# Kernel optimization log

Hardware: AMD Instinct MI355X
Metric: run time of the kernel (lower is better)

The kernel has to match this reference:

```python
import jax, jax.numpy as jnp
import numpy as np

N_NODES = 100000
N_EDGES = 3200000
DIM = 64


def setup_inputs() -> dict:
    key = jax.random.key(0)
    k1, k2, k3, k4 = jax.random.split(key, 4)
    features = jax.random.normal(k1, (N_NODES, DIM), dtype=jnp.float32)
    attn_w = jax.random.normal(k2, (2 * DIM,), dtype=jnp.float32) / np.sqrt(2 * DIM)
    src = jax.random.randint(k3, (N_EDGES,), 0, N_NODES, dtype=jnp.int32)
    dst = jax.random.randint(k4, (N_EDGES,), 0, N_NODES, dtype=jnp.int32)
    return {"features": features, "attn_w": attn_w, "src": src, "dst": dst}


def reference(features, attn_w, src, dst):
    n = features.shape[0]
    d = features.shape[1]
    a_src, a_dst = attn_w[:d], attn_w[d:]
    # Edge attention: leaky_relu(Linear(concat(h_src, h_dst))) == leaky_relu(h_src@a_src + h_dst@a_dst)
    s_src = features @ a_src  # [N]
    s_dst = features @ a_dst  # [N]
    e = jax.nn.leaky_relu(s_src[src] + s_dst[dst], negative_slope=0.01)  # [E]
    # Segment softmax over incoming edges of each destination node
    emax = jax.ops.segment_max(e, dst, num_segments=n)  # [N], -inf for isolated nodes
    ee = jnp.exp(e - emax[dst])  # [E]
    denom = jax.ops.segment_sum(ee, dst, num_segments=n)  # [N]
    alpha = ee / denom[dst]  # [E]
    # Weighted neighbor aggregation (gather src feats, scatter-add into dst)
    h = jax.ops.segment_sum(alpha[:, None] * features[src], dst, num_segments=n)  # [N, D]
    return jax.nn.elu(h)
```

## Files before the change

### kernel.cpp

```cpp
#include <hip/hip_runtime.h>
#include <math.h>

#define DIM 64
#define SCAN_BLOCK 1024
#define NB1 1024
#define TPB2 1024
#define BUCKET_BITS 7
#define BUCKET_SZ 128
#define FB_SZ 64
#define SRC_SHIFT 20
#define CAP 6144
#define CAP2 2560
#define CHUNK 12500
#define STAGE_SZ 12544
#define NSPAN 784

__device__ __forceinline__ float lrelu(float x) { return x > 0.f ? x : 0.01f * x; }
__device__ __forceinline__ float elu(float x)  { return x > 0.f ? x : expm1f(x); }

__global__ __launch_bounds__(TPB2)
void prep_scatter(const float* __restrict__ feat,
                  const float* __restrict__ attn_w,
                  float* __restrict__ s_src,
                  float* __restrict__ s_dst,
                  unsigned short* __restrict__ fbf,
                  int n_nodes,
                  const int* __restrict__ src,
                  const int* __restrict__ dst,
                  int* __restrict__ gcur,
                  int* __restrict__ bpk, int m, int nsb) {
    __shared__ int lh[NB1];
    __shared__ int bnd[NB1];
    __shared__ int cur[NB1];
    __shared__ int span_b[NSPAN];
    __shared__ int stage[STAGE_SZ];
    if (blockIdx.x < nsb) {
        int t = threadIdx.x;
        int lo = blockIdx.x * CHUNK;
        int hi = min(m, lo + CHUNK);
        int cc = hi - lo;
        int nbux = (n_nodes + BUCKET_SZ - 1) >> BUCKET_BITS;
        lh[t] = 0;
        __syncthreads();
        for (int i = lo + t; i < hi; i += TPB2)
            atomicAdd(&lh[dst[i] >> BUCKET_BITS], 1);
        __syncthreads();
        cur[t] = lh[t];
        __syncthreads();
        for (int off = 1; off < NB1; off <<= 1) {
            int u = (t >= off) ? cur[t - off] : 0;
            __syncthreads();
            cur[t] += u;
            __syncthreads();
        }
        int excl = cur[t] - lh[t];
        bnd[t] = excl;
        int c = lh[t];
        int gb = (c > 0) ? atomicAdd(&gcur[t], c) : 0;
        lh[t]  = gb;
        cur[t] = excl;
        __syncthreads();
        if (t < nbux) {
            int s0 = (bnd[t] + 15) >> 4;
            int s1 = (bnd[t + 1] + 15) >> 4;
            for (int s = s0; s < s1; ++s) span_b[s] = t;
        }
        for (int i = lo + t; i < hi; i += TPB2) {
            int d = dst[i];
            int b = d >> BUCKET_BITS;
            int p = atomicAdd(&cur[b], 1);
            stage[p] = src[i] | ((d & (BUCKET_SZ - 1)) << SRC_SHIFT);
        }
        __syncthreads();
        for (int j = t; j < cc; j += TPB2) {
            int bkt = span_b[j >> 4];
            while (bnd[bkt + 1] <= j) ++bkt;
            int pos = lh[bkt] + (j - bnd[bkt]);
            if (pos < CAP)
                bpk[(size_t)bkt * CAP + pos] = stage[j];
        }
        return;
    }
    int gid  = (blockIdx.x - nsb) * blockDim.x + threadIdx.x;
    int node = gid >> 4;
    int lane = gid & 15;
    if (node >= n_nodes) return;
    const float4 f  = *reinterpret_cast<const float4*>(feat + (size_t)node * DIM + lane * 4);
    const float4 as = *reinterpret_cast<const float4*>(attn_w + lane * 4);
    const float4 ad = *reinterpret_cast<const float4*>(attn_w + DIM + lane * 4);
    float ps = f.x * as.x + f.y * as.y + f.z * as.z + f.w * as.w;
    float pd = f.x * ad.x + f.y * ad.y + f.z * ad.z + f.w * ad.w;
    uint b0 = __float_as_uint(f.x), b1 = __float_as_uint(f.y);
    uint b2 = __float_as_uint(f.z), b3 = __float_as_uint(f.w);
    ushort4 h;
    h.x = (unsigned short)((b0 + 0x7FFFu + ((b0 >> 16) & 1u)) >> 16);
    h.y = (unsigned short)((b1 + 0x7FFFu + ((b1 >> 16) & 1u)) >> 16);
    h.z = (unsigned short)((b2 + 0x7FFFu + ((b2 >> 16) & 1u)) >> 16);
    h.w = (unsigned short)((b3 + 0x7FFFu + ((b3 >> 16) & 1u)) >> 16);
    *reinterpret_cast<ushort4*>(fbf + (size_t)node * DIM + lane * 4) = h;
    for (int off = 8; off >= 1; off >>= 1) {
        ps += __shfl_xor(ps, off, 16);
        pd += __shfl_xor(pd, off, 16);
    }
    if (lane == 0) {
        s_src[node] = ps;
        s_dst[node] = pd;
    }
}

__device__ __forceinline__ void bf16x8_acc(uint4 q, float w,
                                           float& a0, float& a1, float& a2, float& a3,
                                           float& a4, float& a5, float& a6, float& a7) {
    a0 += w * __uint_as_float(q.x << 16);
    a1 += w * __uint_as_float(q.x & 0xffff0000u);
    a2 += w * __uint_as_float(q.y << 16);
    a3 += w * __uint_as_float(q.y & 0xffff0000u);
    a4 += w * __uint_as_float(q.z << 16);
    a5 += w * __uint_as_float(q.z & 0xffff0000u);
    a6 += w * __uint_as_float(q.w << 16);
    a7 += w * __uint_as_float(q.w & 0xffff0000u);
}

__global__ __launch_bounds__(256)
void sort_aggregate64(const int* __restrict__ bpk,
                      const int* __restrict__ gcur,
                      const float* __restrict__ s_src,
                      const float* __restrict__ s_dst,
                      const unsigned short* __restrict__ fbf,
                      float* __restrict__ out,
                      int n) {
    __shared__ float sdd[FB_SZ];
    __shared__ int   hist[FB_SZ];
    __shared__ int   offsl[FB_SZ];
    __shared__ int   cur[FB_SZ];
    __shared__ int   sA[FB_SZ];
    __shared__ int   sB[FB_SZ];
    __shared__ int   esrc_l[CAP2];
    __shared__ float w_l[CAP2];
    int f = blockIdx.x, t = threadIdx.x;
    int cb = f >> 1;
    int hb = (f & 1) << 6;
    int base = f * FB_SZ;
    int cnt = min(gcur[cb], CAP);
    const int*  bp  = bpk + (size_t)cb * CAP;
    const uint4* bp4 = reinterpret_cast<const uint4*>(bp);
    int cnt4 = cnt >> 2;
    if (t < FB_SZ) {
        hist[t] = 0;
        int nd = base + t;
        sdd[t] = (nd < n) ? s_dst[nd] : 0.f;
    }
    __syncthreads();
#define HPROC(pk) { int dl7_ = ((pk) >> SRC_SHIFT) & 127; \
    if ((dl7_ & 64) == hb) atomicAdd(&hist[dl7_ & 63], 1); }
    for (int e = t; e < cnt4; e += 256) {
        uint4 v = bp4[e];
        HPROC((int)v.x) HPROC((int)v.y) HPROC((int)v.z) HPROC((int)v.w)
    }
    for (int e = (cnt4 << 2) + t; e < cnt; e += 256)
        HPROC(bp[e])
    __syncthreads();
    if (t < FB_SZ) sA[t] = hist[t];
    __syncthreads();
    {
        int* pin = sA; int* pout = sB;
        for (int off = 1; off < FB_SZ; off <<= 1) {
            if (t < FB_SZ) pout[t] = (t >= off) ? pin[t] + pin[t - off] : pin[t];
            __syncthreads();
            int* tmpp = pin; pin = pout; pout = tmpp;
        }
        if (t < FB_SZ) {
            int excl = min(pin[t] - hist[t], CAP2);
            offsl[t] = excl;
            cur[t] = excl;
        }
    }
    __syncthreads();
#define SPROC(pk) { int dl7_ = ((pk) >> SRC_SHIFT) & 127; \
    if ((dl7_ & 64) == hb) { \
        int sv_ = (pk) & ((1 << SRC_SHIFT) - 1); \
        float w_ = __expf(lrelu(s_src[sv_] + sdd[dl7_ & 63])); \
        int p_ = atomicAdd(&cur[dl7_ & 63], 1); \
        if (p_ < CAP2) { esrc_l[p_] = sv_; w_l[p_] = w_; } } }
    for (int e = t; e < cnt4; e += 256) {
        uint4 v = bp4[e];
        SPROC((int)v.x) SPROC((int)v.y) SPROC((int)v.z) SPROC((int)v.w)
    }
    for (int e = (cnt4 << 2) + t; e < cnt; e += 256)
        SPROC(bp[e])
    __syncthreads();
    int l8 = t & 7, grp = t >> 3;
    const uint4* fv4 = reinterpret_cast<const uint4*>(fbf);
    for (int node = grp; node < FB_SZ; node += 32) {
        int st = offsl[node];
        int en = min(st + hist[node], CAP2);
        float a0 = 0.f, a1 = 0.f, a2 = 0.f, a3 = 0.f;
        float a4 = 0.f, a5 = 0.f, a6 = 0.f, a7 = 0.f;
        float wsum = 0.f;
        int e = st;
        for (; e + 4 <= en; e += 4) {
            int   s0 = esrc_l[e],     s1 = esrc_l[e + 1];
            int   s2 = esrc_l[e + 2], s3 = esrc_l[e + 3];
            float w0 = w_l[e],        w1 = w_l[e + 1];
            float w2 = w_l[e + 2],    w3 = w_l[e + 3];
            uint4 q0 = fv4[(size_t)s0 * 8 + l8];
            uint4 q1 = fv4[(size_t)s1 * 8 + l8];
            uint4 q2 = fv4[(size_t)s2 * 8 + l8];
            uint4 q3 = fv4[(size_t)s3 * 8 + l8];
            wsum += (w0 + w1) + (w2 + w3);
            bf16x8_acc(q0, w0, a0, a1, a2, a3, a4, a5, a6, a7);
            bf16x8_acc(q1, w1, a0, a1, a2, a3, a4, a5, a6, a7);
            bf16x8_acc(q2, w2, a0, a1, a2, a3, a4, a5, a6, a7);
            bf16x8_acc(q3, w3, a0, a1, a2, a3, a4, a5, a6, a7);
        }
        for (; e < en; e++) {
            int   s0 = esrc_l[e];
            float w0 = w_l[e];
            uint4 q0 = fv4[(size_t)s0 * 8 + l8];
            wsum += w0;
            bf16x8_acc(q0, w0, a0, a1, a2, a3, a4, a5, a6, a7);
        }
        int nd = base + node;
        if (nd < n) {
            float inv = (en > st) ? 1.f / wsum : 0.f;
            float4 o1, o2;
            o1.x = elu(a0 * inv); o1.y = elu(a1 * inv);
            o1.z = elu(a2 * inv); o1.w = elu(a3 * inv);
            o2.x = elu(a4 * inv); o2.y = elu(a5 * inv);
            o2.z = elu(a6 * inv); o2.w = elu(a7 * inv);
            float4* orow = reinterpret_cast<float4*>(out + (size_t)nd * DIM + l8 * 8);
            orow[0] = o1;
            orow[1] = o2;
        }
    }
#undef HPROC
#undef SPROC
}

__global__ void compute_scores(const float* __restrict__ feat,
                               const float* __restrict__ attn_w,
                               float* __restrict__ s_src,
                               float* __restrict__ s_dst,
                               int n_nodes) {
    int gid  = blockIdx.x * blockDim.x + threadIdx.x;
    int node = gid >> 4;
    int lane = gid & 15;
    if (node >= n_nodes) return;
    const float4 f  = *reinterpret_cast<const float4*>(feat + (size_t)node * DIM + lane * 4);
    const float4 as = *reinterpret_cast<const float4*>(attn_w + lane * 4);
    const float4 ad = *reinterpret_cast<const float4*>(attn_w + DIM + lane * 4);
    float ps = f.x * as.x + f.y * as.y + f.z * as.z + f.w * as.w;
    float pd = f.x * ad.x + f.y * ad.y + f.z * ad.z + f.w * ad.w;
    for (int off = 8; off >= 1; off >>= 1) {
        ps += __shfl_xor(ps, off, 16);
        pd += __shfl_xor(pd, off, 16);
    }
    if (lane == 0) { s_src[node] = ps; s_dst[node] = pd; }
}

__global__ void scan_level1(const int* __restrict__ in, int* __restrict__ out,
                            int* __restrict__ bsum, int n) {
    __shared__ int tmp[SCAN_BLOCK];
    int t = threadIdx.x;
    int g = blockIdx.x * SCAN_BLOCK + t;
    int v = (g < n) ? in[g] : 0;
    tmp[t] = v;
    __syncthreads();
    for (int off = 1; off < SCAN_BLOCK; off <<= 1) {
        int u = (t >= off) ? tmp[t - off] : 0;
        __syncthreads();
        tmp[t] += u;
        __syncthreads();
    }
    if (g < n) out[g] = tmp[t] - v;
    if (t == SCAN_BLOCK - 1) bsum[blockIdx.x] = tmp[t];
}

__global__ void scan_level2(int* __restrict__ bsum, int nb) {
    __shared__ int tmp[SCAN_BLOCK];
    int t = threadIdx.x;
    int v = (t < nb) ? bsum[t] : 0;
    tmp[t] = v;
    __syncthreads();
    for (int off = 1; off < SCAN_BLOCK; off <<= 1) {
        int u = (t >= off) ? tmp[t - off] : 0;
        __syncthreads();
        tmp[t] += u;
        __syncthreads();
    }
    if (t < nb) bsum[t] = tmp[t] - v;
}

__global__ void scan_level3(int* __restrict__ out, const int* __restrict__ bsum,
                            int n) {
    int g = blockIdx.x * SCAN_BLOCK + threadIdx.x;
    if (g < n) out[g] += bsum[blockIdx.x];
}

__global__ void degree_rank(const int* __restrict__ dst, int* __restrict__ deg,
                            int* __restrict__ rank, int m) {
    int i = blockIdx.x * blockDim.x + threadIdx.x;
    if (i >= m) return;
    rank[i] = atomicAdd(&deg[dst[i]], 1);
}

__global__ void scatter_src(const int* __restrict__ src, const int* __restrict__ dst,
                            const int* __restrict__ rank, const int* __restrict__ offs,
                            int* __restrict__ esrc, int m) {
    int i = blockIdx.x * blockDim.x + threadIdx.x;
    if (i >= m) return;
    esrc[offs[dst[i]] + rank[i]] = src[i];
}

__global__ void aggregate_f32(const int* __restrict__ esrc,
                              const int* __restrict__ offs,
                              const int* __restrict__ deg,
                              const float* __restrict__ s_src,
                              const float* __restrict__ s_dst,
                              const float* __restrict__ feat,
                              float* __restrict__ out, int n) {
    int gid  = blockIdx.x * blockDim.x + threadIdx.x;
    int node = gid >> 4;
    int lane = gid & 15;
    if (node >= n) return;
    int start = offs[node];
    int cnt   = deg[node];
    float sdd = s_dst[node];
    const float4* fv = reinterpret_cast<const float4*>(feat);
    float4 acc = {0.f, 0.f, 0.f, 0.f};
    float wsum = 0.f;
    for (int e = 0; e < cnt; e++) {
        int s0 = esrc[start + e];
        float w0 = __expf(lrelu(s_src[s0] + sdd));
        float4 f0 = fv[s0 * 16 + lane];
        wsum += w0;
        acc.x += w0 * f0.x; acc.y += w0 * f0.y;
        acc.z += w0 * f0.z; acc.w += w0 * f0.w;
    }
    float inv = (cnt > 0) ? 1.f / wsum : 0.f;
    float4 o;
    o.x = elu(acc.x * inv); o.y = elu(acc.y * inv);
    o.z = elu(acc.z * inv); o.w = elu(acc.w * inv);
    reinterpret_cast<float4*>(out)[node * 16 + lane] = o;
}

extern "C" void kernel_launch(void* const* d_in, const int* in_sizes, int n_in,
                              void* d_out, int out_size, void* d_ws, size_t ws_size,
                              hipStream_t stream) {
    const float* feat   = (const float*)d_in[0];
    const float* attn_w = (const float*)d_in[1];
    const int*   src    = (const int*)d_in[2];
    const int*   dst    = (const int*)d_in[3];

    const int n = in_sizes[0] / DIM;
    const int m = in_sizes[2];

    float* out = (float*)d_out;

    const int nbux = (n + BUCKET_SZ - 1) >> BUCKET_BITS;
    const int nfb  = (n + FB_SZ - 1) / FB_SZ;

    float* s_src = (float*)d_ws;
    float* s_dst = s_src + n;
    unsigned short* fbf = (unsigned short*)(s_dst + n);
    int*   gcur  = (int*)(fbf + (size_t)n * DIM);
    int*   bpk   = gcur + NB1;
    size_t need  = ((size_t)(2 + DIM / 2) * n + NB1 + (size_t)nbux * CAP)
                   * sizeof(int);

    if (ws_size >= need && nbux <= NB1) {
        hipMemsetAsync(gcur, 0, (size_t)NB1 * sizeof(int), stream);

        int nsb = (m + CHUNK - 1) / CHUNK;
        int PB  = (n * 16 + TPB2 - 1) / TPB2;
        prep_scatter<<<nsb + PB, TPB2, 0, stream>>>(
            feat, attn_w, s_src, s_dst, fbf, n, src, dst, gcur, bpk, m, nsb);

        sort_aggregate64<<<nfb, 256, 0, stream>>>(
            bpk, gcur, s_src, s_dst, fbf, out, n);
    } else {
        int* deg2  = (int*)(s_dst + n);
        int* offs2 = deg2 + n;
        int* bsum2 = offs2 + n;
        int* rank  = bsum2 + SCAN_BLOCK;
        int* esr2  = rank + m;
        int threads = n * 16;
        compute_scores<<<(threads + 255) / 256, 256, 0, stream>>>(
            feat, attn_w, s_src, s_dst, n);
        hipMemsetAsync(deg2, 0, (size_t)n * sizeof(int), stream);
        degree_rank<<<(m + 255) / 256, 256, 0, stream>>>(dst, deg2, rank, m);
        int nb2 = (n + SCAN_BLOCK - 1) / SCAN_BLOCK;
        scan_level1<<<nb2, SCAN_BLOCK, 0, stream>>>(deg2, offs2, bsum2, n);
        scan_level2<<<1, SCAN_BLOCK, 0, stream>>>(bsum2, nb2);
        scan_level3<<<nb2, SCAN_BLOCK, 0, stream>>>(offs2, bsum2, n);
        scatter_src<<<(m + 255) / 256, 256, 0, stream>>>(src, dst, rank, offs2, esr2, m);
        aggregate_f32<<<(threads + 255) / 256, 256, 0, stream>>>(
            esr2, offs2, deg2, s_src, s_dst, feat, out, n);
    }
}
```

Baseline: 187.8 us.

## Bucket edges per 64-node block instead of 128-node buckets

The scatter pass now buckets edges by 64-node blocks, one bucket per aggregation block, using 2048 local histogram bins and a two-per-thread scan. Before, each 128-node bucket was read by two aggregation blocks, each keeping only half the edges. Now every aggregation block reads only its own edges, roughly halving bucket traffic and discarded histogram/sort work. In exchange the scatter kernel has more bins, more global atomics and finer-grained, more scattered writes.

```diff
diff --git a/kernel.cpp b/kernel.cpp
--- a/kernel.cpp
+++ b/kernel.cpp
@@ -3,14 +3,12 @@
 
 #define DIM 64
 #define SCAN_BLOCK 1024
-#define NB1 1024
+#define NBF 2048
 #define TPB2 1024
-#define BUCKET_BITS 7
-#define BUCKET_SZ 128
+#define FB_BITS 6
 #define FB_SZ 64
 #define SRC_SHIFT 20
-#define CAP 6144
-#define CAP2 2560
+#define CAPF 2560
 #define CHUNK 12500
 #define STAGE_SZ 12544
 #define NSPAN 784
@@ -29,9 +27,9 @@
                   const int* __restrict__ dst,
                   int* __restrict__ gcur,
                   int* __restrict__ bpk, int m, int nsb) {
-    __shared__ int lh[NB1];
-    __shared__ int bnd[NB1];
-    __shared__ int cur[NB1];
+    __shared__ int lh[NBF];
+    __shared__ int bnd[NBF];
+    __shared__ int cur[NBF];
     __shared__ int span_b[NSPAN];
     __shared__ int stage[STAGE_SZ];
     if (blockIdx.x < nsb) {
@@ -39,45 +37,51 @@
         int lo = blockIdx.x * CHUNK;
         int hi = min(m, lo + CHUNK);
         int cc = hi - lo;
-        int nbux = (n_nodes + BUCKET_SZ - 1) >> BUCKET_BITS;
+        int nfb = (n_nodes + FB_SZ - 1) >> FB_BITS;
         lh[t] = 0;
+        lh[t + TPB2] = 0;
         __syncthreads();
         for (int i = lo + t; i < hi; i += TPB2)
-            atomicAdd(&lh[dst[i] >> BUCKET_BITS], 1);
-        __syncthreads();
-        cur[t] = lh[t];
-        __syncthreads();
-        for (int off = 1; off < NB1; off <<= 1) {
-            int u = (t >= off) ? cur[t - off] : 0;
+            atomicAdd(&lh[dst[i] >> FB_BITS], 1);
+        __syncthreads();
+        int a0 = lh[2 * t], a1 = lh[2 * t + 1];
+        int ps = a0 + a1;
+        stage[t] = ps;
+        __syncthreads();
+        for (int off = 1; off < TPB2; off <<= 1) {
+            int u = (t >= off) ? stage[t - off] : 0;
             __syncthreads();
-            cur[t] += u;
+            stage[t] += u;
             __syncthreads();
         }
-        int excl = cur[t] - lh[t];
-        bnd[t] = excl;
-        int c = lh[t];
-        int gb = (c > 0) ? atomicAdd(&gcur[t], c) : 0;
-        lh[t]  = gb;
-        cur[t] = excl;
-        __syncthreads();
-        if (t < nbux) {
-            int s0 = (bnd[t] + 15) >> 4;
-            int s1 = (bnd[t + 1] + 15) >> 4;
-            for (int s = s0; s < s1; ++s) span_b[s] = t;
+        int pexcl = stage[t] - ps;
+        bnd[2 * t]     = pexcl;
+        bnd[2 * t + 1] = pexcl + a0;
+        int gb0 = (a0 > 0) ? atomicAdd(&gcur[2 * t], a0) : 0;
+        int gb1 = (a1 > 0) ? atomicAdd(&gcur[2 * t + 1], a1) : 0;
+        lh[2 * t]     = gb0;
+        lh[2 * t + 1] = gb1;
+        cur[2 * t]     = pexcl;
+        cur[2 * t + 1] = pexcl + a0;
+        __syncthreads();
+        for (int b = t; b < nfb; b += TPB2) {
+            int s0 = (bnd[b] + 15) >> 4;
+            int s1 = (bnd[b + 1] + 15) >> 4;
+            for (int s = s0; s < s1; ++s) span_b[s] = b;
         }
         for (int i = lo + t; i < hi; i += TPB2) {
             int d = dst[i];
-            int b = d >> BUCKET_BITS;
+            int b = d >> FB_BITS;
             int p = atomicAdd(&cur[b], 1);
-            stage[p] = src[i] | ((d & (BUCKET_SZ - 1)) << SRC_SHIFT);
+            stage[p] = src[i] | ((d & (FB_SZ - 1)) << SRC_SHIFT);
         }
         __syncthreads();
         for (int j = t; j < cc; j += TPB2) {
             int bkt = span_b[j >> 4];
             while (bnd[bkt + 1] <= j) ++bkt;
             int pos = lh[bkt] + (j - bnd[bkt]);
-            if (pos < CAP)
-                bpk[(size_t)bkt * CAP + pos] = stage[j];
+            if (pos < CAPF)
+                bpk[(size_t)bkt * CAPF + pos] = stage[j];
         }
         return;
     }
@@ -135,14 +139,12 @@
     __shared__ int   cur[FB_SZ];
     __shared__ int   sA[FB_SZ];
     __shared__ int   sB[FB_SZ];
-    __shared__ int   esrc_l[CAP2];
-    __shared__ float w_l[CAP2];
+    __shared__ int   esrc_l[CAPF];
+    __shared__ float w_l[CAPF];
     int f = blockIdx.x, t = threadIdx.x;
-    int cb = f >> 1;
-    int hb = (f & 1) << 6;
     int base = f * FB_SZ;
-    int cnt = min(gcur[cb], CAP);
-    const int*  bp  = bpk + (size_t)cb * CAP;
+    int cnt = min(gcur[f], CAPF);
+    const int*  bp  = bpk + (size_t)f * CAPF;
     const uint4* bp4 = reinterpret_cast<const uint4*>(bp);
     int cnt4 = cnt >> 2;
     if (t < FB_SZ) {
@@ -151,8 +153,7 @@
         sdd[t] = (nd < n) ? s_dst[nd] : 0.f;
     }
     __syncthreads();
-#define HPROC(pk) { int dl7_ = ((pk) >> SRC_SHIFT) & 127; \
-    if ((dl7_ & 64) == hb) atomicAdd(&hist[dl7_ & 63], 1); }
+#define HPROC(pk) atomicAdd(&hist[((pk) >> SRC_SHIFT) & (FB_SZ - 1)], 1);
     for (int e = t; e < cnt4; e += 256) {
         uint4 v = bp4[e];
         HPROC((int)v.x) HPROC((int)v.y) HPROC((int)v.z) HPROC((int)v.w)
@@ -170,18 +171,18 @@
             int* tmpp = pin; pin = pout; pout = tmpp;
         }
         if (t < FB_SZ) {
-            int excl = min(pin[t] - hist[t], CAP2);
+            int excl = min(pin[t] - hist[t], CAPF);
             offsl[t] = excl;
             cur[t] = excl;
         }
     }
     __syncthreads();
-#define SPROC(pk) { int dl7_ = ((pk) >> SRC_SHIFT) & 127; \
-    if ((dl7_ & 64) == hb) { \
+#define SPROC(pk) { \
+        int dl_ = ((pk) >> SRC_SHIFT) & (FB_SZ - 1); \
         int sv_ = (pk) & ((1 << SRC_SHIFT) - 1); \
-        float w_ = __expf(lrelu(s_src[sv_] + sdd[dl7_ & 63])); \
-        int p_ = atomicAdd(&cur[dl7_ & 63], 1); \
-        if (p_ < CAP2) { esrc_l[p_] = sv_; w_l[p_] = w_; } } }
+        float w_ = __expf(lrelu(s_src[sv_] + sdd[dl_])); \
+        int p_ = atomicAdd(&cur[dl_], 1); \
+        if (p_ < CAPF) { esrc_l[p_] = sv_; w_l[p_] = w_; } }
     for (int e = t; e < cnt4; e += 256) {
         uint4 v = bp4[e];
         SPROC((int)v.x) SPROC((int)v.y) SPROC((int)v.z) SPROC((int)v.w)
@@ -193,7 +194,7 @@
     const uint4* fv4 = reinterpret_cast<const uint4*>(fbf);
     for (int node = grp; node < FB_SZ; node += 32) {
         int st = offsl[node];
-        int en = min(st + hist[node], CAP2);
+        int en = min(st + hist[node], CAPF);
         float a0 = 0.f, a1 = 0.f, a2 = 0.f, a3 = 0.f;
         float a4 = 0.f, a5 = 0.f, a6 = 0.f, a7 = 0.f;
         float wsum = 0.f;
@@ -357,19 +358,18 @@
 
     float* out = (float*)d_out;
 
-    const int nbux = (n + BUCKET_SZ - 1) >> BUCKET_BITS;
-    const int nfb  = (n + FB_SZ - 1) / FB_SZ;
+    const int nfb = (n + FB_SZ - 1) >> FB_BITS;
 
     float* s_src = (float*)d_ws;
     float* s_dst = s_src + n;
     unsigned short* fbf = (unsigned short*)(s_dst + n);
     int*   gcur  = (int*)(fbf + (size_t)n * DIM);
-    int*   bpk   = gcur + NB1;
-    size_t need  = ((size_t)(2 + DIM / 2) * n + NB1 + (size_t)nbux * CAP)
+    int*   bpk   = gcur + NBF;
+    size_t need  = ((size_t)(2 + DIM / 2) * n + NBF + (size_t)nfb * CAPF)
                    * sizeof(int);
 
-    if (ws_size >= need && nbux <= NB1) {
-        hipMemsetAsync(gcur, 0, (size_t)NB1 * sizeof(int), stream);
+    if (ws_size >= need && nfb < NBF) {
+        hipMemsetAsync(gcur, 0, (size_t)NBF * sizeof(int), stream);
 
         int nsb = (m + CHUNK - 1) / CHUNK;
         int PB  = (n * 16 + TPB2 - 1) / TPB2;
```

Result: slower. 199.2 us (+6.0%).
